# Kernel tuning notes

Measured on AMD Instinct MI355X. Metric: run time of the kernel, lower is better.

## Reference

```python
import jax, jax.numpy as jnp
import numpy as np

BATCH, N_IN, N_OUT, DEGREE = 128, 2048, 1024, 15
EPSILON = 1.0
TEMPERATURE = 0.1
NEG_FILL = -1000000000.0


def setup_inputs() -> dict:
    key = jax.random.key(0)
    k1, k2, k3 = jax.random.split(key, 3)
    x = jax.random.normal(k1, (BATCH, N_IN), dtype=jnp.float32)
    weights = jax.random.normal(k2, (N_OUT, N_IN), dtype=jnp.float32) * 0.02
    # buffer: (rand(n_out, n_in) < degree/n_in).float()
    synaptic_mask = (jax.random.uniform(k3, (N_OUT, N_IN)) < DEGREE / N_IN).astype(jnp.float32)
    return {"x": x, "weights": weights, "synaptic_mask": synaptic_mask}


def reference(x, weights, synaptic_mask):
    n_in = x.shape[1]
    # torch.median returns the LOWER of the two middle values for even n:
    # sorted index (n-1)//2
    consensus = jnp.sort(x, axis=1)[:, (n_in - 1) // 2][:, None]  # [B, 1]
    gate = (jnp.abs(x - consensus) < EPSILON).astype(x.dtype)      # [B, n_in]
    gated_x = x * gate                                             # [B, n_in]
    # dense broadcast-add: [B, n_out, n_in]
    combined = gated_x[:, None, :] + weights[None, :, :]
    masked_z = jnp.where(synaptic_mask == 0.0, NEG_FILL, combined)
    return TEMPERATURE * jax.nn.logsumexp(masked_z / TEMPERATURE, axis=2)  # [B, n_out]
```

## Files before the change

### kernel.cpp

```cpp
#include <hip/hip_runtime.h>
#include <math.h>

#define BATCH 128
#define N_IN 2048
#define N_OUT 1024
#define MAXK 40
#define BCAP 64
#define TEMP 0.1f
#define INV_TEMP 10.0f
#define NEG_FILL -1.0e9f
#define WLO -0.1875f
#define WHI 0.1875f
#define BINSCALE 682.6666666f

__device__ __forceinline__ unsigned int f2key(float f) {
    unsigned int b = __float_as_uint(f);
    return (b & 0x80000000u) ? ~b : (b | 0x80000000u);
}
__device__ __forceinline__ float key2f(unsigned int u) {
    unsigned int b = (u & 0x80000000u) ? (u & 0x7FFFFFFFu) : ~u;
    return __uint_as_float(b);
}

__global__ __launch_bounds__(256) void k_prep(const float* __restrict__ x,
                                              const float* __restrict__ w,
                                              const float* __restrict__ msk,
                                              int* __restrict__ cnt,
                                              int2* __restrict__ listsT,
                                              float* __restrict__ med) {
    __shared__ unsigned int hist[256];
    __shared__ unsigned int wsum4[4];
    __shared__ unsigned int sel[2];
    __shared__ float sbin[BCAP];
    __shared__ int s_nb;
    __shared__ float s_med;
    __shared__ int sidx[MAXK];

    const int tid = threadIdx.x;
    const int lane = tid & 63;
    const int wwid = tid >> 6;
    const int bid = (int)blockIdx.x;

    if (bid < BATCH) {
        const int b = bid;
        const float4* xr = (const float4*)(x + (size_t)b * N_IN);
        float4 va = xr[tid], vb = xr[tid + 256];
        float vals[8] = {va.x, va.y, va.z, va.w, vb.x, vb.y, vb.z, vb.w};

        hist[tid] = 0;
        if (tid == 0) s_nb = 0;
        __syncthreads();

        int cb = 0;
#pragma unroll
        for (int j = 0; j < 8; ++j) {
            float v = vals[j];
            cb += (v < WLO) ? 1 : 0;
            if (v >= WLO && v < WHI) {
                int bin = (int)((v - WLO) * BINSCALE);
                bin = (bin > 255) ? 255 : bin;
                atomicAdd(&hist[bin], 1u);
            }
        }
        int sb = cb;
#pragma unroll
        for (int off = 1; off < 64; off <<= 1) sb += __shfl_xor(sb, off, 64);
        if (lane == 0) wsum4[wwid] = (unsigned int)sb;
        __syncthreads();
        const int c_lo = (int)(wsum4[0] + wsum4[1] + wsum4[2] + wsum4[3]);
        const int R = (N_IN - 1) / 2 - c_lo;

        unsigned int hv = hist[tid];
        unsigned int sv = hv;
#pragma unroll
        for (int off = 1; off < 64; off <<= 1) {
            unsigned int t = __shfl_up(sv, off, 64);
            if (lane >= off) sv += t;
        }
        __syncthreads();
        if (lane == 63) wsum4[wwid] = sv;
        if (tid == 0) sel[0] = 0xFFFFFFFFu;
        __syncthreads();
        unsigned int base = 0;
        for (int ww = 0; ww < wwid; ++ww) base += wsum4[ww];
        const unsigned int incl = sv + base;
        const unsigned int excl = incl - hv;
        const int n_c = (int)(wsum4[0] + wsum4[1] + wsum4[2] + wsum4[3]);
        if (R >= 0 && R < n_c && (unsigned int)R >= excl && (unsigned int)R < incl) {
            sel[0] = (unsigned int)tid;
            sel[1] = (unsigned int)R - excl;
        }
        __syncthreads();

        bool fast_ok = (R >= 0 && R < n_c && sel[0] != 0xFFFFFFFFu);
        if (fast_ok) {
            const int B = (int)sel[0];
            const int r2 = (int)sel[1];
#pragma unroll
            for (int j = 0; j < 8; ++j) {
                float v = vals[j];
                if (v >= WLO && v < WHI) {
                    int bin = (int)((v - WLO) * BINSCALE);
                    bin = (bin > 255) ? 255 : bin;
                    if (bin == B) {
                        int p = atomicAdd(&s_nb, 1);
                        if (p < BCAP) sbin[p] = v;
                    }
                }
            }
            __syncthreads();
            const int nb = s_nb;
            if (nb <= BCAP) {
                if (tid < nb) {
                    float v = sbin[tid];
                    int nlt = 0, neq = 0;
                    for (int j = 0; j < nb; ++j) {
                        float u = sbin[j];
                        nlt += (u < v) ? 1 : 0;
                        neq += (u == v) ? 1 : 0;
                    }
                    if (nlt <= r2 && r2 < nlt + neq) s_med = v;
                }
            } else {
                fast_ok = false;
            }
            __syncthreads();
        }
        if (!fast_ok) {
            unsigned int prefix = 0;
            unsigned int k = (N_IN - 1) / 2;
            for (int pos = 24; pos >= 0; pos -= 8) {
                hist[tid] = 0;
                __syncthreads();
                const unsigned int hmask = (pos == 24) ? 0u : (0xFFFFFFFFu << (pos + 8));
#pragma unroll
                for (int j = 0; j < 8; ++j) {
                    unsigned int u = f2key(vals[j]);
                    if ((u & hmask) == (prefix & hmask))
                        atomicAdd(&hist[(u >> pos) & 0xFFu], 1u);
                }
                __syncthreads();
                unsigned int v = hist[tid];
                unsigned int s2 = v;
#pragma unroll
                for (int off = 1; off < 64; off <<= 1) {
                    unsigned int t = __shfl_up(s2, off, 64);
                    if (lane >= off) s2 += t;
                }
                if (lane == 63) wsum4[wwid] = s2;
                __syncthreads();
                unsigned int bs = 0;
                for (int ww = 0; ww < wwid; ++ww) bs += wsum4[ww];
                const unsigned int inc2 = s2 + bs;
                const unsigned int exc2 = inc2 - v;
                if (k >= exc2 && k < inc2) {
                    sel[0] = (unsigned int)tid;
                    sel[1] = k - exc2;
                }
                __syncthreads();
                prefix |= sel[0] << pos;
                k = sel[1];
                __syncthreads();
            }
            if (tid == 0) s_med = key2f(prefix);
            __syncthreads();
        }
        if (tid == 0) med[b] = s_med;
    } else {
        const int o = bid - BATCH;
        const float4* mr = (const float4*)(msk + (size_t)o * N_IN);
        float4 ma = mr[tid], mb = mr[tid + 256];
        float mv[8] = {ma.x, ma.y, ma.z, ma.w, mb.x, mb.y, mb.z, mb.w};

        int myc = 0;
#pragma unroll
        for (int j = 0; j < 8; ++j) myc += (mv[j] != 0.0f);

        int sv = myc;
#pragma unroll
        for (int off = 1; off < 64; off <<= 1) {
            int t = __shfl_up(sv, off, 64);
            if (lane >= off) sv += t;
        }
        if (lane == 63) wsum4[wwid] = (unsigned int)sv;
        __syncthreads();
        int base = 0;
        for (int ww = 0; ww < wwid; ++ww) base += (int)wsum4[ww];
        const int incl = sv + base;
        const int excl = incl - myc;
        const int c_tot = (int)(wsum4[0] + wsum4[1] + wsum4[2] + wsum4[3]);
        if (tid == 0) cnt[o] = c_tot;

        int p = excl;
#pragma unroll
        for (int j = 0; j < 8; ++j) {
            if (mv[j] != 0.0f) {
                if (p < MAXK) {
                    int idx = (j < 4) ? 4 * tid + j : 1024 + 4 * tid + (j - 4);
                    sidx[p] = idx;
                }
                ++p;
            }
        }
        __syncthreads();

        const int cc = (c_tot < MAXK) ? c_tot : MAXK;
        if (tid < cc) {
            const int idx = sidx[tid];
            const float wv = w[(size_t)o * N_IN + idx];
            listsT[tid * N_OUT + o] = make_int2(idx, __float_as_int(wv));
        }
    }
}

__global__ __launch_bounds__(256) void k_lse(const float* __restrict__ x,
                                             const float* __restrict__ medv,
                                             const int* __restrict__ cnt,
                                             const int2* __restrict__ listsT,
                                             const float* __restrict__ w,
                                             const float* __restrict__ msk,
                                             float* __restrict__ out) {
    __shared__ float sgx[N_IN];
    const int b = blockIdx.x >> 2;
    const int oq = blockIdx.x & 3;
    const int tid = threadIdx.x;

    const float med = medv[b];
    const float4* xr = (const float4*)(x + (size_t)b * N_IN);
    float4 va = xr[tid], vb = xr[tid + 256];
    float4 ga, gb;
    ga.x = (fabsf(va.x - med) < 1.0f) ? va.x : 0.0f;
    ga.y = (fabsf(va.y - med) < 1.0f) ? va.y : 0.0f;
    ga.z = (fabsf(va.z - med) < 1.0f) ? va.z : 0.0f;
    ga.w = (fabsf(va.w - med) < 1.0f) ? va.w : 0.0f;
    gb.x = (fabsf(vb.x - med) < 1.0f) ? vb.x : 0.0f;
    gb.y = (fabsf(vb.y - med) < 1.0f) ? vb.y : 0.0f;
    gb.z = (fabsf(vb.z - med) < 1.0f) ? vb.z : 0.0f;
    gb.w = (fabsf(vb.w - med) < 1.0f) ? vb.w : 0.0f;
    ((float4*)sgx)[tid] = ga;
    ((float4*)sgx)[tid + 256] = gb;
    __syncthreads();

    const int o = oq * 256 + tid;
    const int c = cnt[o];
    float res;
    if (c == 0) {
        res = NEG_FILL;
    } else if (c <= MAXK) {
        int2 e = listsT[o];
        float m = (sgx[e.x] + __int_as_float(e.y)) * INV_TEMP;
        float s = 1.0f;
        for (int j = 1; j < c; ++j) {
            e = listsT[j * N_OUT + o];
            float v = (sgx[e.x] + __int_as_float(e.y)) * INV_TEMP;
            float mn = fmaxf(m, v);
            s = s * __expf(m - mn) + __expf(v - mn);
            m = mn;
        }
        res = TEMP * (m + __logf(s));
    } else {
        const float* mr = msk + (size_t)o * N_IN;
        const float* wr = w + (size_t)o * N_IN;
        float m = -INFINITY, s = 0.0f;
        for (int i = 0; i < N_IN; ++i) {
            if (mr[i] != 0.0f) {
                float v = (sgx[i] + wr[i]) * INV_TEMP;
                float mn = fmaxf(m, v);
                s = s * __expf(m - mn) + __expf(v - mn);
                m = mn;
            }
        }
        res = TEMP * (m + __logf(s));
    }
    out[(size_t)b * N_OUT + o] = res;
}

extern "C" void kernel_launch(void* const* d_in, const int* in_sizes, int n_in,
                              void* d_out, int out_size, void* d_ws, size_t ws_size,
                              hipStream_t stream) {
    const float* x = (const float*)d_in[0];
    const float* w = (const float*)d_in[1];
    const float* msk = (const float*)d_in[2];
    float* out = (float*)d_out;

    int* cnt = (int*)d_ws;
    int2* listsT = (int2*)(cnt + N_OUT);
    float* med = (float*)(listsT + (size_t)MAXK * N_OUT);

    hipLaunchKernelGGL(k_prep, dim3(BATCH + N_OUT), dim3(256), 0, stream,
                       x, w, msk, cnt, listsT, med);
    hipLaunchKernelGGL(k_lse, dim3(BATCH * 4), dim3(256), 0, stream,
                       x, med, cnt, listsT, w, msk, out);
}
```

Before: 16.33 us.

## Write sparse lists directly from prep and gate x on the fly in lse

In the prep kernel, each thread now loads the weights for its own nonzero mask entries and writes the list entries straight to global memory. This removes the shared index buffer, a barrier and the dependent gather from w. In the lse kernel, the shared-memory staging of the gated x row and its barrier are gone, and x is gathered directly from global memory (cache) with the gate applied per element. This trades a coalesced row load for scattered, cached global reads, in exchange for fewer synchronisation points.

```diff
diff --git a/kernel.cpp b/kernel.cpp
--- a/kernel.cpp
+++ b/kernel.cpp
@@ -34,7 +34,6 @@
     __shared__ float sbin[BCAP];
     __shared__ int s_nb;
     __shared__ float s_med;
-    __shared__ int sidx[MAXK];
 
     const int tid = threadIdx.x;
     const int lane = tid & 63;
@@ -171,6 +170,14 @@
         const float4* mr = (const float4*)(msk + (size_t)o * N_IN);
         float4 ma = mr[tid], mb = mr[tid + 256];
         float mv[8] = {ma.x, ma.y, ma.z, ma.w, mb.x, mb.y, mb.z, mb.w};
+        const float* wr = w + (size_t)o * N_IN;
+
+        float wv[8];
+#pragma unroll
+        for (int j = 0; j < 8; ++j) {
+            const int idx = (j < 4) ? 4 * tid + j : 1024 + 4 * tid + (j - 4);
+            wv[j] = (mv[j] != 0.0f) ? wr[idx] : 0.0f;
+        }
 
         int myc = 0;
 #pragma unroll
@@ -188,27 +195,18 @@
         for (int ww = 0; ww < wwid; ++ww) base += (int)wsum4[ww];
         const int incl = sv + base;
         const int excl = incl - myc;
-        const int c_tot = (int)(wsum4[0] + wsum4[1] + wsum4[2] + wsum4[3]);
-        if (tid == 0) cnt[o] = c_tot;
+        if (tid == 255) cnt[o] = incl;
 
         int p = excl;
 #pragma unroll
         for (int j = 0; j < 8; ++j) {
             if (mv[j] != 0.0f) {
                 if (p < MAXK) {
-                    int idx = (j < 4) ? 4 * tid + j : 1024 + 4 * tid + (j - 4);
-                    sidx[p] = idx;
+                    const int idx = (j < 4) ? 4 * tid + j : 1024 + 4 * tid + (j - 4);
+                    listsT[p * N_OUT + o] = make_int2(idx, __float_as_int(wv[j]));
                 }
                 ++p;
             }
-        }
-        __syncthreads();
-
-        const int cc = (c_tot < MAXK) ? c_tot : MAXK;
-        if (tid < cc) {
-            const int idx = sidx[tid];
-            const float wv = w[(size_t)o * N_IN + idx];
-            listsT[tid * N_OUT + o] = make_int2(idx, __float_as_int(wv));
         }
     }
 }
@@ -220,39 +218,29 @@
                                              const float* __restrict__ w,
                                              const float* __restrict__ msk,
                                              float* __restrict__ out) {
-    __shared__ float sgx[N_IN];
     const int b = blockIdx.x >> 2;
     const int oq = blockIdx.x & 3;
     const int tid = threadIdx.x;
 
     const float med = medv[b];
-    const float4* xr = (const float4*)(x + (size_t)b * N_IN);
-    float4 va = xr[tid], vb = xr[tid + 256];
-    float4 ga, gb;
-    ga.x = (fabsf(va.x - med) < 1.0f) ? va.x : 0.0f;
-    ga.y = (fabsf(va.y - med) < 1.0f) ? va.y : 0.0f;
-    ga.z = (fabsf(va.z - med) < 1.0f) ? va.z : 0.0f;
-    ga.w = (fabsf(va.w - med) < 1.0f) ? va.w : 0.0f;
-    gb.x = (fabsf(vb.x - med) < 1.0f) ? vb.x : 0.0f;
-    gb.y = (fabsf(vb.y - med) < 1.0f) ? vb.y : 0.0f;
-    gb.z = (fabsf(vb.z - med) < 1.0f) ? vb.z : 0.0f;
-    gb.w = (fabsf(vb.w - med) < 1.0f) ? vb.w : 0.0f;
-    ((float4*)sgx)[tid] = ga;
-    ((float4*)sgx)[tid + 256] = gb;
-    __syncthreads();
-
+    const float* __restrict__ xrow = x + (size_t)b * N_IN;
     const int o = oq * 256 + tid;
     const int c = cnt[o];
+
     float res;
     if (c == 0) {
         res = NEG_FILL;
     } else if (c <= MAXK) {
         int2 e = listsT[o];
-        float m = (sgx[e.x] + __int_as_float(e.y)) * INV_TEMP;
+        float xv = xrow[e.x];
+        float g = (fabsf(xv - med) < 1.0f) ? xv : 0.0f;
+        float m = (g + __int_as_float(e.y)) * INV_TEMP;
         float s = 1.0f;
         for (int j = 1; j < c; ++j) {
             e = listsT[j * N_OUT + o];
-            float v = (sgx[e.x] + __int_as_float(e.y)) * INV_TEMP;
+            xv = xrow[e.x];
+            g = (fabsf(xv - med) < 1.0f) ? xv : 0.0f;
+            float v = (g + __int_as_float(e.y)) * INV_TEMP;
             float mn = fmaxf(m, v);
             s = s * __expf(m - mn) + __expf(v - mn);
             m = mn;
@@ -264,7 +252,9 @@
         float m = -INFINITY, s = 0.0f;
         for (int i = 0; i < N_IN; ++i) {
             if (mr[i] != 0.0f) {
-                float v = (sgx[i] + wr[i]) * INV_TEMP;
+                float xv = xrow[i];
+                float g = (fabsf(xv - med) < 1.0f) ? xv : 0.0f;
+                float v = (g + wr[i]) * INV_TEMP;
                 float mn = fmaxf(m, v);
                 s = s * __expf(m - mn) + __expf(v - mn);
                 m = mn;
```

Result: slower. 21.86 us (+33.9%).
